# Optimization experiments

Hardware: AMD Instinct MI355X
Metric: run time of the kernel (lower is better)

Reference implementation:

```python
import jax, jax.numpy as jnp
import numpy as np

# Fixed geometry from the module's voxel_dict
VOXEL = np.array([0.32, 0.32, 6.0], dtype=np.float32)
PC_MIN = np.array([-74.88, -74.88, -2.0], dtype=np.float32)
PC_MAX = np.array([74.88, 74.88, 4.0], dtype=np.float32)
NX, NY, NZ = 468, 468, 1          # round((max-min)/voxel) per axis
CANVAS = NZ * NY * NX             # 219024 voxels (batch_size = 1)
OFFSET = VOXEL / 2.0 + PC_MIN     # x/y/z_offset from __init__


def setup_inputs() -> dict:
    key = jax.random.key(0)
    k1, k2, k3, k4 = jax.random.split(key, 4)
    N = 400000
    # points uniformly inside the point-cloud range (dynamic voxelization keeps all)
    xyz = jax.random.uniform(k1, (N, 3), dtype=jnp.float32) * (PC_MAX - PC_MIN) * 0.999 + PC_MIN
    extra = jax.random.normal(k2, (N, 2), dtype=jnp.float32)
    points = jnp.concatenate([xyz, extra], axis=1)          # [N, 5]
    W1 = jax.random.normal(k3, (11, 64), dtype=jnp.float32) * 0.05
    W2 = jax.random.normal(k4, (128, 64), dtype=jnp.float32) * 0.05
    return {"points": points, "W1": W1, "W2": W2}


def _flat_voxel_index(xyz):
    # dynamic voxelization: integer voxel coord per point, (z, y, x) ordering
    c = jnp.floor((xyz - PC_MIN) / VOXEL).astype(jnp.int32)
    cx = jnp.clip(c[:, 0], 0, NX - 1)
    cy = jnp.clip(c[:, 1], 0, NY - 1)
    cz = jnp.clip(c[:, 2], 0, NZ - 1)
    flat = cz * (NY * NX) + cy * NX + cx                    # canvas index as in map_voxel_center_to_point
    return flat, cx, cy, cz


def reference(points, W1, W2):
    xyz = points[:, :3]
    flat, cx, cy, cz = _flat_voxel_index(xyz)

    # DynamicScatter mean (cluster_scatter)
    cnt = jax.ops.segment_sum(jnp.ones((points.shape[0],), jnp.float32), flat, num_segments=CANVAS)
    vsum = jax.ops.segment_sum(points, flat, num_segments=CANVAS)
    vmean = vsum / jnp.maximum(cnt, 1.0)[:, None]           # [CANVAS, 5]
    pmean = vmean[flat]                                     # gather voxel mean to points

    f_cluster = xyz - pmean[:, :3]
    centers = jnp.stack([cx, cy, cz], axis=1).astype(jnp.float32) * VOXEL + OFFSET
    f_center = xyz - centers
    features = jnp.concatenate([points, f_cluster, f_center], axis=-1)   # [N, 11]

    occ = (cnt > 0)[:, None]

    # PFN layer 1: Linear(bias=False) + ReLU, then scatter-max to voxels
    pf1 = jax.nn.relu(features @ W1)                        # [N, 64]
    v1 = jax.ops.segment_max(pf1, flat, num_segments=CANVAS)
    v1 = jnp.where(occ, v1, 0.0)                            # zero empty voxels (replaces -inf)

    # gather voxel max back to points, concat, PFN layer 2
    feat2 = jnp.concatenate([pf1, v1[flat]], axis=1)        # [N, 128]
    pf2 = jax.nn.relu(feat2 @ W2)                           # [N, 64]
    v2 = jax.ops.segment_max(pf2, flat, num_segments=CANVAS)
    v2 = jnp.where(occ, v2, 0.0)                            # [CANVAS, 64] dense voxel features
    return v2
```

## Files before the change

kernel.cpp:

```cpp
#include <hip/hip_runtime.h>

#define NXc 468
#define NYc 468
#define CANVASc (468 * 468)
#define NPTS 400000
#define RUN 16
#define NRUNS (NPTS / RUN)
#define GPTS ((NPTS + 255) / 256)
#define GVOX ((CANVASc + 255) / 256)
#define GBND (NRUNS / 4)

#define PCMIN_X (-74.88f)
#define PCMIN_Y (-74.88f)
#define VOX_X 0.32f
#define VOX_Y 0.32f
#define OFF_X (-74.72f)
#define OFF_Y (-74.72f)
#define OFF_Z (1.0f)

typedef __attribute__((ext_vector_type(8))) short v8s;
typedef __attribute__((ext_vector_type(4))) float v4f;

static_assert(sizeof(__bf16) == 2, "bf16 must be 2 bytes");

__device__ __forceinline__ int rli(int x, int p) {
    return __builtin_amdgcn_readlane(x, p);
}
__device__ __forceinline__ float rlf(float x, int p) {
    return __int_as_float(__builtin_amdgcn_readlane(__float_as_int(x), p));
}

__device__ __forceinline__ void split8(const float* f, v8s& h, v8s& l) {
    #pragma unroll
    for (int i = 0; i < 8; i += 2) {
        __bf16 h0 = (__bf16)f[i];
        __bf16 h1 = (__bf16)f[i + 1];
        h[i]     = __builtin_bit_cast(short, h0);
        h[i + 1] = __builtin_bit_cast(short, h1);
        float l0 = f[i]     - (float)h0;
        float l1 = f[i + 1] - (float)h1;
        l[i]     = __builtin_bit_cast(short, (__bf16)l0);
        l[i + 1] = __builtin_bit_cast(short, (__bf16)l1);
    }
}

__device__ __forceinline__ int voxel_cell(float x, float y, int& cx, int& cy) {
    cx = (int)floorf((x - PCMIN_X) / VOX_X);
    cy = (int)floorf((y - PCMIN_Y) / VOX_Y);
    cx = min(max(cx, 0), NXc - 1);
    cy = min(max(cy, 0), NYc - 1);
    return cy * NXc + cx;
}

__device__ __forceinline__ void kw_body(int tid,
                                        const float* __restrict__ W1,
                                        const float* __restrict__ W2,
                                        v8s* __restrict__ w1frag,
                                        v8s* __restrict__ w2frag) {
    if (tid < 1024) {
        int f = tid >> 6, lane = tid & 63;
        int t = f >> 2, c = f & 3;
        int q = lane >> 4, n = lane & 15;
        float v[8];
        #pragma unroll
        for (int i = 0; i < 8; i++) v[i] = W2[(c * 32 + q * 8 + i) * 64 + t * 16 + n];
        v8s h, l;
        split8(v, h, l);
        w2frag[(f * 2 + 0) * 64 + lane] = h;
        w2frag[(f * 2 + 1) * 64 + lane] = l;
    } else if (tid < 1280) {
        int f = (tid - 1024) >> 6, lane = (tid - 1024) & 63;
        int q = lane >> 4, n = lane & 15;
        float v[8];
        #pragma unroll
        for (int i = 0; i < 8; i++) {
            int k = q * 8 + i;
            v[i] = (k < 11) ? W1[k * 64 + f * 16 + n] : 0.f;
        }
        v8s h, l;
        split8(v, h, l);
        w1frag[(f * 2 + 0) * 64 + lane] = h;
        w1frag[(f * 2 + 1) * 64 + lane] = l;
    }
}

__global__ __launch_bounds__(256) void k_stats(const float* __restrict__ pts,
                                               int* __restrict__ cnt,
                                               int* __restrict__ rankb,
                                               int* __restrict__ cellu,
                                               const float* __restrict__ W1,
                                               const float* __restrict__ W2,
                                               v8s* __restrict__ w1frag,
                                               v8s* __restrict__ w2frag) {
    int b = blockIdx.x;
    if (b >= GPTS) {
        kw_body((b - GPTS) * 256 + threadIdx.x, W1, W2, w1frag, w2frag);
        return;
    }
    int i = b * 256 + threadIdx.x;
    if (i >= NPTS) return;
    float x = pts[i * 5 + 0], y = pts[i * 5 + 1];
    int cx, cy;
    int fl = voxel_cell(x, y, cx, cy);
    rankb[i] = atomicAdd(&cnt[fl], 1);
    cellu[i] = cx | (cy << 16);
}

__global__ __launch_bounds__(256) void k_alloc(const int* __restrict__ cnt,
                                               int* __restrict__ cursor,
                                               int* __restrict__ gcur,
                                               float4* __restrict__ out4) {
    int v = blockIdx.x * 256 + threadIdx.x;
    int lane = threadIdx.x & 63;
    int c = (v < CANVASc) ? cnt[v] : 0;
    int scan = c;
    #pragma unroll
    for (int off = 1; off < 64; off <<= 1) {
        int t = __shfl_up(scan, off, 64);
        if (lane >= off) scan += t;
    }
    int total = __shfl(scan, 63, 64);
    int base = 0;
    if (lane == 0 && total > 0) base = atomicAdd(gcur, total);
    base = __shfl(base, 0, 64);
    if (v < CANVASc) {
        cursor[v] = base + scan - c;
        if (c == 0) {
            float4 z = make_float4(0.f, 0.f, 0.f, 0.f);
            float4* o = out4 + (size_t)v * 16;
            #pragma unroll
            for (int i = 0; i < 16; i++) o[i] = z;
        }
    }
}

__device__ __forceinline__ void gather_pt(const float* __restrict__ pts, int pi,
                                          float4& A, float& e1) {
    const float* pp = pts + (size_t)pi * 5;
    __builtin_memcpy(&A, pp, 16);
    e1 = pp[4];
}

__global__ __launch_bounds__(256) void k_scatter(const float* __restrict__ pts,
                                                 const int* __restrict__ cursor,
                                                 const int* __restrict__ rankb,
                                                 const int* __restrict__ cellu,
                                                 float4* __restrict__ pos4,
                                                 float* __restrict__ e1b,
                                                 int* __restrict__ cellb) {
    int i = blockIdx.x * 256 + threadIdx.x;
    if (i >= NPTS) return;
    float4 A; float e1;
    gather_pt(pts, i, A, e1);
    int cell = cellu[i];
    int cx = cell & 0xFFFF, cy = cell >> 16;
    int fl = cy * NXc + cx;
    int pos = cursor[fl] + rankb[i];
    pos4[pos] = A;
    e1b[pos] = e1;
    cellb[pos] = cell;
}

__global__ __launch_bounds__(256) void kS(const int* __restrict__ cnt,
                                          const int* __restrict__ cursor,
                                          const float4* __restrict__ pos4,
                                          const float* __restrict__ e1b,
                                          const int* __restrict__ cellb,
                                          const float* __restrict__ W1,
                                          float4* __restrict__ vmc,
                                          float* __restrict__ v1c,
                                          float* __restrict__ out) {
    int j = threadIdx.x & 63;
    int wslot = threadIdx.x >> 6;
    int w = blockIdx.x * 4 + wslot;
    if (w == 0 || w >= NRUNS) return;
    int bb = w * RUN;
    int ca = cellb[bb - 1], cb0 = cellb[bb];
    if (ca != cb0) return;
    int cx = ca & 0xFFFF, cy = ca >> 16;
    int v = cy * NXc + cx;
    int c = cnt[v];
    int start = cursor[v];
    out[(size_t)v * 64 + j] = 0.f;

    float sx = 0.f, sy = 0.f, sz = 0.f;
    for (int pb = 0; pb < c; pb += 64) {
        int pc = min(c - pb, 64);
        if (j < pc) {
            float4 A = pos4[start + pb + j];
            sx += A.x; sy += A.y; sz += A.z;
        }
    }
    #pragma unroll
    for (int off = 1; off < 64; off <<= 1) {
        sx += __shfl_xor(sx, off, 64);
        sy += __shfl_xor(sy, off, 64);
        sz += __shfl_xor(sz, off, 64);
    }
    float inv = 1.0f / (float)c;
    float mx = sx * inv, my = sy * inv, mz = sz * inv;
    if (j == 0) vmc[w] = make_float4(mx, my, mz, 0.f);

    float wgt[11];
    #pragma unroll
    for (int k = 0; k < 11; k++) wgt[k] = W1[k * 64 + j];
    float vmax = 0.f;
    for (int pb = 0; pb < c; pb += 64) {
        int pc = min(c - pb, 64);
        float f[11];
        #pragma unroll
        for (int k = 0; k < 11; k++) f[k] = 0.f;
        if (j < pc) {
            int idx = start + pb + j;
            float4 A = pos4[idx];
            float e1 = e1b[idx];
            int cell = cellb[idx];
            int ccx = cell & 0xFFFF, ccy = cell >> 16;
            f[0] = A.x; f[1] = A.y; f[2] = A.z; f[3] = A.w; f[4] = e1;
            f[5] = A.x - mx; f[6] = A.y - my; f[7] = A.z - mz;
            f[8] = A.x - (ccx * VOX_X + OFF_X);
            f[9] = A.y - (ccy * VOX_Y + OFF_Y);
            f[10] = A.z - OFF_Z;
        }
        for (int p = 0; p < pc; p++) {
            float acc = 0.f;
            #pragma unroll
            for (int k = 0; k < 11; k++)
                acc = fmaf(rlf(f[k], p), wgt[k], acc);
            vmax = fmaxf(vmax, acc);
        }
    }
    v1c[(size_t)w * 64 + j] = vmax;
}

struct PtRegs {
    float4 A;
    float  e1, fcx, fcy, fcz;
    float  mx, my, mz;
    int    vx;
};

#define PSTR 68

__device__ __forceinline__ void phase1_mfma(float (*s_pf)[PSTR], const PtRegs& P,
                                            const v8s* __restrict__ w1frag, int j) {
    if (j < RUN) {
        float* row = s_pf[j];
        row[0] = P.A.x; row[1] = P.A.y; row[2] = P.A.z; row[3] = P.A.w; row[4] = P.e1;
        row[5] = P.A.x - P.mx; row[6] = P.A.y - P.my; row[7] = P.A.z - P.mz;
        row[8] = P.fcx; row[9] = P.fcy; row[10] = P.fcz;
        #pragma unroll
        for (int t = 11; t < 16; t++) row[t] = 0.f;
    }
    __builtin_amdgcn_wave_barrier();

    const int m = j & 15, q = j >> 4;
    v8s fh = {0,0,0,0,0,0,0,0}, fl_ = {0,0,0,0,0,0,0,0};
    if (q < 2) {
        float f8[8];
        #pragma unroll
        for (int i = 0; i < 8; i++) f8[i] = s_pf[m][q * 8 + i];
        split8(f8, fh, fl_);
    }
    v4f d[4];
    #pragma unroll
    for (int t = 0; t < 4; t++) {
        v8s bh = w1frag[(t * 2 + 0) * 64 + j];
        v8s bl = w1frag[(t * 2 + 1) * 64 + j];
        v4f acc = {0.f, 0.f, 0.f, 0.f};
        acc = __builtin_amdgcn_mfma_f32_16x16x32_bf16(fh,  bh, acc, 0, 0, 0);
        acc = __builtin_amdgcn_mfma_f32_16x16x32_bf16(fl_, bh, acc, 0, 0, 0);
        acc = __builtin_amdgcn_mfma_f32_16x16x32_bf16(fh,  bl, acc, 0, 0, 0);
        d[t] = acc;
    }
    __builtin_amdgcn_wave_barrier();
    #pragma unroll
    for (int t = 0; t < 4; t++)
        #pragma unroll
        for (int r = 0; r < 4; r++)
            s_pf[q * 4 + r][t * 16 + m] = fmaxf(d[t][r], 0.f);
    __builtin_amdgcn_wave_barrier();
}

__global__ __launch_bounds__(256) void kB(const float4* __restrict__ pos4,
                                          const float* __restrict__ e1b,
                                          const int* __restrict__ cellb,
                                          const float4* __restrict__ vmc,
                                          const v8s* __restrict__ w1frag,
                                          const v8s* __restrict__ w2frag,
                                          const float* __restrict__ v1c,
                                          float* __restrict__ out) {
    __shared__ float s_pf[4][RUN][PSTR];
    int wslot = threadIdx.x >> 6;
    int wave = blockIdx.x * 4 + wslot;
    int j = threadIdx.x & 63;
    int base = wave * RUN;

    const int m = j & 15, q = j >> 4;

    int idx = -1;
    if (j < RUN) idx = base + j;
    else if (j == 16) idx = (base + RUN < NPTS) ? base + RUN : -1;
    else if (j == 17) idx = base - 1;

    int cell = 0, vx = -1;
    if (idx >= 0) {
        cell = cellb[idx];
        vx = (cell >> 16) * NXc + (cell & 0xFFFF);
    }
    float4 A = make_float4(0.f, 0.f, 0.f, 0.f);
    float e1 = 0.f;
    if (j < RUN) { A = pos4[idx]; e1 = e1b[idx]; }

    const int first = rli(vx, 0), last = rli(vx, RUN - 1);
    const bool firstExt = (rli(vx, 17) == first);
    const bool lastExt  = (rli(vx, 16) == last);

    int vx_m = __builtin_amdgcn_ds_bpermute(m << 2, vx);
    int vx_prev = __shfl_up(vx, 1, 64);
    unsigned long long B =
        __ballot((j < RUN) && ((j == 0) || (vx != vx_prev)));
    int s_seg = 63 - __builtin_clzll(B & ((2ULL << m) - 1ULL));
    int e_seg = m + 1 + (int)__builtin_ctzll((B | (1ULL << RUN)) >> (m + 1));
    const bool fext_m = (vx_m == first && firstExt);
    const bool ext_m = fext_m || (vx_m == last && lastExt);
    const int bidx = fext_m ? wave : (wave + 1);

    PtRegs P;
    P.A = A; P.e1 = e1; P.vx = vx;
    P.mx = P.my = P.mz = P.fcx = P.fcy = P.fcz = 0.f;
    if (j < RUN) {
        if (ext_m) {
            float4 mv = vmc[bidx];
            P.mx = mv.x; P.my = mv.y; P.mz = mv.z;
        } else {
            float sx = 0.f, sy = 0.f, sz = 0.f;
            for (int p = s_seg; p < e_seg; p++) {
                sx += __shfl(A.x, p, 64);
                sy += __shfl(A.y, p, 64);
                sz += __shfl(A.z, p, 64);
            }
            float inv = 1.0f / (float)(e_seg - s_seg);
            P.mx = sx * inv; P.my = sy * inv; P.mz = sz * inv;
        }
        int cx = cell & 0xFFFF, cy = cell >> 16;
        P.fcx = A.x - (cx * VOX_X + OFF_X);
        P.fcy = A.y - (cy * VOX_Y + OFF_Y);
        P.fcz = A.z - OFF_Z;
    }

    phase1_mfma(s_pf[wslot], P, w1frag, j);

    float vf[16];
    if (ext_m) {
        const float* vr = v1c + (size_t)bidx * 64 + q * 8;
        #pragma unroll
        for (int c = 0; c < 2; c++)
            #pragma unroll
            for (int i = 0; i < 8; i++) vf[c * 8 + i] = vr[c * 32 + i];
    }

    v8s ah[4], al[4];
    #pragma unroll
    for (int c = 0; c < 2; c++) {
        float f[8];
        #pragma unroll
        for (int i = 0; i < 8; i++) f[i] = s_pf[wslot][m][c * 32 + q * 8 + i];
        split8(f, ah[c], al[c]);
    }
    if (!ext_m) {
        #pragma unroll
        for (int i = 0; i < 16; i++) vf[i] = 0.f;
        for (int p = s_seg; p < e_seg; p++) {
            const float* row = s_pf[wslot][p];
            float4 a0 = *(const float4*)&row[q * 8];
            float4 a1 = *(const float4*)&row[q * 8 + 4];
            float4 b0 = *(const float4*)&row[32 + q * 8];
            float4 b1 = *(const float4*)&row[32 + q * 8 + 4];
            vf[0] = fmaxf(vf[0], a0.x);  vf[1] = fmaxf(vf[1], a0.y);
            vf[2] = fmaxf(vf[2], a0.z);  vf[3] = fmaxf(vf[3], a0.w);
            vf[4] = fmaxf(vf[4], a1.x);  vf[5] = fmaxf(vf[5], a1.y);
            vf[6] = fmaxf(vf[6], a1.z);  vf[7] = fmaxf(vf[7], a1.w);
            vf[8] = fmaxf(vf[8], b0.x);  vf[9] = fmaxf(vf[9], b0.y);
            vf[10] = fmaxf(vf[10], b0.z); vf[11] = fmaxf(vf[11], b0.w);
            vf[12] = fmaxf(vf[12], b1.x); vf[13] = fmaxf(vf[13], b1.y);
            vf[14] = fmaxf(vf[14], b1.z); vf[15] = fmaxf(vf[15], b1.w);
        }
    }
    split8(vf + 0, ah[2], al[2]);
    split8(vf + 8, ah[3], al[3]);
    __builtin_amdgcn_wave_barrier();

    #pragma unroll
    for (int t = 0; t < 4; t++) {
        v8s bh[4], bl[4];
        #pragma unroll
        for (int c = 0; c < 4; c++) {
            bh[c] = w2frag[((t * 4 + c) * 2 + 0) * 64 + j];
            bl[c] = w2frag[((t * 4 + c) * 2 + 1) * 64 + j];
        }
        v4f acc = {0.f, 0.f, 0.f, 0.f};
        #pragma unroll
        for (int c = 0; c < 4; c++) {
            acc = __builtin_amdgcn_mfma_f32_16x16x32_bf16(ah[c], bh[c], acc, 0, 0, 0);
            acc = __builtin_amdgcn_mfma_f32_16x16x32_bf16(al[c], bh[c], acc, 0, 0, 0);
            acc = __builtin_amdgcn_mfma_f32_16x16x32_bf16(ah[c], bl[c], acc, 0, 0, 0);
        }
        #pragma unroll
        for (int r = 0; r < 4; r++) s_pf[wslot][q * 4 + r][t * 16 + m] = acc[r];
    }
    __builtin_amdgcn_wave_barrier();

    int vprev = first;
    float smax = -3.4e38f;
    for (int p = 0; p < RUN; p++) {
        int vp = rli(vx, p);
        if (vp != vprev) {
            float r = fmaxf(smax, 0.f);
            size_t o = (size_t)vprev * 64 + j;
            bool ua = (vprev == first && firstExt) || (vprev == last && lastExt);
            if (ua) atomicMax((int*)out + o, __float_as_int(r));
            else out[o] = r;
            vprev = vp; smax = -3.4e38f;
        }
        smax = fmaxf(smax, s_pf[wslot][p][j]);
    }
    {
        float r = fmaxf(smax, 0.f);
        size_t o = (size_t)vprev * 64 + j;
        bool ua = (vprev == first && firstExt) || (vprev == last && lastExt);
        if (ua) atomicMax((int*)out + o, __float_as_int(r));
        else out[o] = r;
    }
}

extern "C" void kernel_launch(void* const* d_in, const int* in_sizes, int n_in,
                              void* d_out, int out_size, void* d_ws, size_t ws_size,
                              hipStream_t stream) {
    const float* pts = (const float*)d_in[0];
    const float* W1  = (const float*)d_in[1];
    const float* W2  = (const float*)d_in[2];
    float* out = (float*)d_out;

    float4* vmc    = (float4*)d_ws;
    float*  v1c    = (float*)(vmc + NRUNS);
    float4* pos4   = (float4*)(v1c + (size_t)NRUNS * 64);
    float*  e1b    = (float*)(pos4 + NPTS);
    int*    cellb  = (int*)(e1b + NPTS);
    int*    rankb  = cellb + NPTS;
    int*    cellu  = rankb + NPTS;
    v8s*    w2frag = (v8s*)(cellu + NPTS);
    v8s*    w1frag = w2frag + 2048;
    int*    cnt    = (int*)(w1frag + 512);
    int*    gcur   = cnt + CANVASc;
    int*    cursor = gcur + 1;

    hipMemsetAsync(cnt, 0, (size_t)(CANVASc + 1) * 4, stream);

    k_stats  <<<GPTS + 5, 256, 0, stream>>>(pts, cnt, rankb, cellu,
                                            W1, W2, w1frag, w2frag);
    k_alloc  <<<GVOX, 256, 0, stream>>>(cnt, cursor, gcur, (float4*)out);
    k_scatter<<<GPTS, 256, 0, stream>>>(pts, cursor, rankb, cellu,
                                        pos4, e1b, cellb);
    kS       <<<GBND, 256, 0, stream>>>(cnt, cursor, pos4, e1b, cellb,
                                        W1, vmc, v1c, out);
    kB       <<<NRUNS / 4, 256, 0, stream>>>(pos4, e1b, cellb, vmc, w1frag,
                                             w2frag, v1c, out);
}
```

Baseline: 223.4 us.

## Process two 16-point runs per wave in kB to reuse weight fragments

After: 218.0 us. 1.03x faster.

```diff
diff --git a/kernel.cpp b/kernel.cpp
--- a/kernel.cpp
+++ b/kernel.cpp
@@ -5,10 +5,13 @@
 #define CANVASc (468 * 468)
 #define NPTS 400000
 #define RUN 16
+#define WPTS 32
 #define NRUNS (NPTS / RUN)
+#define NWAVE (NPTS / WPTS)
 #define GPTS ((NPTS + 255) / 256)
 #define GVOX ((CANVASc + 255) / 256)
 #define GBND (NRUNS / 4)
+#define GKB  (NWAVE / 4)
 
 #define PCMIN_X (-74.88f)
 #define PCMIN_Y (-74.88f)
@@ -233,54 +236,7 @@
     v1c[(size_t)w * 64 + j] = vmax;
 }
 
-struct PtRegs {
-    float4 A;
-    float  e1, fcx, fcy, fcz;
-    float  mx, my, mz;
-    int    vx;
-};
-
 #define PSTR 68
-
-__device__ __forceinline__ void phase1_mfma(float (*s_pf)[PSTR], const PtRegs& P,
-                                            const v8s* __restrict__ w1frag, int j) {
-    if (j < RUN) {
-        float* row = s_pf[j];
-        row[0] = P.A.x; row[1] = P.A.y; row[2] = P.A.z; row[3] = P.A.w; row[4] = P.e1;
-        row[5] = P.A.x - P.mx; row[6] = P.A.y - P.my; row[7] = P.A.z - P.mz;
-        row[8] = P.fcx; row[9] = P.fcy; row[10] = P.fcz;
-        #pragma unroll
-        for (int t = 11; t < 16; t++) row[t] = 0.f;
-    }
-    __builtin_amdgcn_wave_barrier();
-
-    const int m = j & 15, q = j >> 4;
-    v8s fh = {0,0,0,0,0,0,0,0}, fl_ = {0,0,0,0,0,0,0,0};
-    if (q < 2) {
-        float f8[8];
-        #pragma unroll
-        for (int i = 0; i < 8; i++) f8[i] = s_pf[m][q * 8 + i];
-        split8(f8, fh, fl_);
-    }
-    v4f d[4];
-    #pragma unroll
-    for (int t = 0; t < 4; t++) {
-        v8s bh = w1frag[(t * 2 + 0) * 64 + j];
-        v8s bl = w1frag[(t * 2 + 1) * 64 + j];
-        v4f acc = {0.f, 0.f, 0.f, 0.f};
-        acc = __builtin_amdgcn_mfma_f32_16x16x32_bf16(fh,  bh, acc, 0, 0, 0);
-        acc = __builtin_amdgcn_mfma_f32_16x16x32_bf16(fl_, bh, acc, 0, 0, 0);
-        acc = __builtin_amdgcn_mfma_f32_16x16x32_bf16(fh,  bl, acc, 0, 0, 0);
-        d[t] = acc;
-    }
-    __builtin_amdgcn_wave_barrier();
-    #pragma unroll
-    for (int t = 0; t < 4; t++)
-        #pragma unroll
-        for (int r = 0; r < 4; r++)
-            s_pf[q * 4 + r][t * 16 + m] = fmaxf(d[t][r], 0.f);
-    __builtin_amdgcn_wave_barrier();
-}
 
 __global__ __launch_bounds__(256) void kB(const float4* __restrict__ pos4,
                                           const float* __restrict__ e1b,
@@ -290,18 +246,19 @@
                                           const v8s* __restrict__ w2frag,
                                           const float* __restrict__ v1c,
                                           float* __restrict__ out) {
-    __shared__ float s_pf[4][RUN][PSTR];
+    __shared__ float s_pf[4][WPTS][PSTR];
     int wslot = threadIdx.x >> 6;
     int wave = blockIdx.x * 4 + wslot;
     int j = threadIdx.x & 63;
-    int base = wave * RUN;
+    int base = wave * WPTS;
 
     const int m = j & 15, q = j >> 4;
+    float (*spf)[PSTR] = s_pf[wslot];
 
     int idx = -1;
-    if (j < RUN) idx = base + j;
-    else if (j == 16) idx = (base + RUN < NPTS) ? base + RUN : -1;
-    else if (j == 17) idx = base - 1;
+    if (j < WPTS) idx = base + j;
+    else if (j == 32) idx = (base + WPTS < NPTS) ? base + WPTS : -1;
+    else if (j == 33) idx = base - 1;
 
     int cell = 0, vx = -1;
     if (idx >= 0) {
@@ -310,85 +267,160 @@
     }
     float4 A = make_float4(0.f, 0.f, 0.f, 0.f);
     float e1 = 0.f;
-    if (j < RUN) { A = pos4[idx]; e1 = e1b[idx]; }
-
-    const int first = rli(vx, 0), last = rli(vx, RUN - 1);
-    const bool firstExt = (rli(vx, 17) == first);
-    const bool lastExt  = (rli(vx, 16) == last);
-
-    int vx_m = __builtin_amdgcn_ds_bpermute(m << 2, vx);
+    if (j < WPTS) { A = pos4[idx]; e1 = e1b[idx]; }
+
+    const int first0 = rli(vx, 0),  last0 = rli(vx, 15);
+    const int first1 = rli(vx, 16), last1 = rli(vx, 31);
+    const bool firstExt0 = (rli(vx, 33) == first0);
+    const bool midExt    = (first1 == last0);
+    const bool lastExt0  = midExt;
+    const bool firstExt1 = midExt;
+    const bool lastExt1  = (rli(vx, 32) == last1);
+
     int vx_prev = __shfl_up(vx, 1, 64);
     unsigned long long B =
-        __ballot((j < RUN) && ((j == 0) || (vx != vx_prev)));
-    int s_seg = 63 - __builtin_clzll(B & ((2ULL << m) - 1ULL));
-    int e_seg = m + 1 + (int)__builtin_ctzll((B | (1ULL << RUN)) >> (m + 1));
-    const bool fext_m = (vx_m == first && firstExt);
-    const bool ext_m = fext_m || (vx_m == last && lastExt);
-    const int bidx = fext_m ? wave : (wave + 1);
-
-    PtRegs P;
-    P.A = A; P.e1 = e1; P.vx = vx;
-    P.mx = P.my = P.mz = P.fcx = P.fcy = P.fcz = 0.f;
-    if (j < RUN) {
-        if (ext_m) {
-            float4 mv = vmc[bidx];
-            P.mx = mv.x; P.my = mv.y; P.mz = mv.z;
+        __ballot((j < WPTS) && ((j == 0) || (j == 16) || (vx != vx_prev)));
+
+    const int P1 = 16 + m;
+    int s0_ = 63 - __builtin_clzll(B & ((2ULL << m) - 1ULL));
+    int e0_ = m + 1 + (int)__builtin_ctzll((B | (1ULL << WPTS)) >> (m + 1));
+    int s1_ = 63 - __builtin_clzll(B & ((2ULL << P1) - 1ULL));
+    int e1_ = P1 + 1 + (int)__builtin_ctzll((B | (1ULL << WPTS)) >> (P1 + 1));
+
+    int vxm0 = __builtin_amdgcn_ds_bpermute(m << 2, vx);
+    int vxm1 = __builtin_amdgcn_ds_bpermute(P1 << 2, vx);
+    const bool fext0 = (vxm0 == first0 && firstExt0);
+    const bool ext0  = fext0 || (vxm0 == last0 && lastExt0);
+    const int  bidx0 = fext0 ? (2 * wave) : (2 * wave + 1);
+    const bool fext1 = (vxm1 == first1 && firstExt1);
+    const bool ext1  = fext1 || (vxm1 == last1 && lastExt1);
+    const int  bidx1 = fext1 ? (2 * wave + 1) : (2 * wave + 2);
+
+    float mx = 0.f, my = 0.f, mz = 0.f, fcx = 0.f, fcy = 0.f, fcz = 0.f;
+    if (j < WPTS) {
+        bool own_ext  = (j < 16) ? ext0 : ext1;
+        int  own_bidx = (j < 16) ? bidx0 : bidx1;
+        int  own_s    = (j < 16) ? s0_ : s1_;
+        int  own_e    = (j < 16) ? e0_ : e1_;
+        if (own_ext) {
+            float4 mv = vmc[own_bidx];
+            mx = mv.x; my = mv.y; mz = mv.z;
         } else {
             float sx = 0.f, sy = 0.f, sz = 0.f;
-            for (int p = s_seg; p < e_seg; p++) {
+            for (int p = own_s; p < own_e; p++) {
                 sx += __shfl(A.x, p, 64);
                 sy += __shfl(A.y, p, 64);
                 sz += __shfl(A.z, p, 64);
             }
-            float inv = 1.0f / (float)(e_seg - s_seg);
-            P.mx = sx * inv; P.my = sy * inv; P.mz = sz * inv;
+            float inv = 1.0f / (float)(own_e - own_s);
+            mx = sx * inv; my = sy * inv; mz = sz * inv;
         }
         int cx = cell & 0xFFFF, cy = cell >> 16;
-        P.fcx = A.x - (cx * VOX_X + OFF_X);
-        P.fcy = A.y - (cy * VOX_Y + OFF_Y);
-        P.fcz = A.z - OFF_Z;
-    }
-
-    phase1_mfma(s_pf[wslot], P, w1frag, j);
-
-    float vf[16];
-    if (ext_m) {
-        const float* vr = v1c + (size_t)bidx * 64 + q * 8;
+        fcx = A.x - (cx * VOX_X + OFF_X);
+        fcy = A.y - (cy * VOX_Y + OFF_Y);
+        fcz = A.z - OFF_Z;
+    }
+
+    if (j < WPTS) {
+        float* row = spf[j];
+        row[0] = A.x; row[1] = A.y; row[2] = A.z; row[3] = A.w; row[4] = e1;
+        row[5] = A.x - mx; row[6] = A.y - my; row[7] = A.z - mz;
+        row[8] = fcx; row[9] = fcy; row[10] = fcz;
+        #pragma unroll
+        for (int t = 11; t < 16; t++) row[t] = 0.f;
+    }
+    __builtin_amdgcn_wave_barrier();
+
+    v8s fh0 = {0,0,0,0,0,0,0,0}, fl0 = {0,0,0,0,0,0,0,0};
+    v8s fh1 = {0,0,0,0,0,0,0,0}, fl1 = {0,0,0,0,0,0,0,0};
+    if (q < 2) {
+        float f8[8];
+        #pragma unroll
+        for (int i = 0; i < 8; i++) f8[i] = spf[m][q * 8 + i];
+        split8(f8, fh0, fl0);
+        #pragma unroll
+        for (int i = 0; i < 8; i++) f8[i] = spf[16 + m][q * 8 + i];
+        split8(f8, fh1, fl1);
+    }
+    v4f d0[4], d1[4];
+    #pragma unroll
+    for (int t = 0; t < 4; t++) {
+        v8s bh = w1frag[(t * 2 + 0) * 64 + j];
+        v8s bl = w1frag[(t * 2 + 1) * 64 + j];
+        v4f a0 = {0.f, 0.f, 0.f, 0.f}, a1 = {0.f, 0.f, 0.f, 0.f};
+        a0 = __builtin_amdgcn_mfma_f32_16x16x32_bf16(fh0, bh, a0, 0, 0, 0);
+        a0 = __builtin_amdgcn_mfma_f32_16x16x32_bf16(fl0, bh, a0, 0, 0, 0);
+        a0 = __builtin_amdgcn_mfma_f32_16x16x32_bf16(fh0, bl, a0, 0, 0, 0);
+        a1 = __builtin_amdgcn_mfma_f32_16x16x32_bf16(fh1, bh, a1, 0, 0, 0);
+        a1 = __builtin_amdgcn_mfma_f32_16x16x32_bf16(fl1, bh, a1, 0, 0, 0);
+        a1 = __builtin_amdgcn_mfma_f32_16x16x32_bf16(fh1, bl, a1, 0, 0, 0);
+        d0[t] = a0; d1[t] = a1;
+    }
+    __builtin_amdgcn_wave_barrier();
+    #pragma unroll
+    for (int t = 0; t < 4; t++)
+        #pragma unroll
+        for (int r = 0; r < 4; r++) {
+            spf[q * 4 + r][t * 16 + m]      = fmaxf(d0[t][r], 0.f);
+            spf[16 + q * 4 + r][t * 16 + m] = fmaxf(d1[t][r], 0.f);
+        }
+    __builtin_amdgcn_wave_barrier();
+
+    float vf0[16], vf1[16];
+    if (ext0) {
+        const float* vr = v1c + (size_t)bidx0 * 64 + q * 8;
         #pragma unroll
         for (int c = 0; c < 2; c++)
             #pragma unroll
-            for (int i = 0; i < 8; i++) vf[c * 8 + i] = vr[c * 32 + i];
-    }
-
-    v8s ah[4], al[4];
+            for (int i = 0; i < 8; i++) vf0[c * 8 + i] = vr[c * 32 + i];
+    }
+    if (ext1) {
+        const float* vr = v1c + (size_t)bidx1 * 64 + q * 8;
+        #pragma unroll
+        for (int c = 0; c < 2; c++)
+            #pragma unroll
+            for (int i = 0; i < 8; i++) vf1[c * 8 + i] = vr[c * 32 + i];
+    }
+
+    v8s ah0[4], al0[4], ah1[4], al1[4];
     #pragma unroll
     for (int c = 0; c < 2; c++) {
         float f[8];
         #pragma unroll
-        for (int i = 0; i < 8; i++) f[i] = s_pf[wslot][m][c * 32 + q * 8 + i];
-        split8(f, ah[c], al[c]);
-    }
-    if (!ext_m) {
-        #pragma unroll
-        for (int i = 0; i < 16; i++) vf[i] = 0.f;
-        for (int p = s_seg; p < e_seg; p++) {
-            const float* row = s_pf[wslot][p];
-            float4 a0 = *(const float4*)&row[q * 8];
-            float4 a1 = *(const float4*)&row[q * 8 + 4];
-            float4 b0 = *(const float4*)&row[32 + q * 8];
-            float4 b1 = *(const float4*)&row[32 + q * 8 + 4];
-            vf[0] = fmaxf(vf[0], a0.x);  vf[1] = fmaxf(vf[1], a0.y);
-            vf[2] = fmaxf(vf[2], a0.z);  vf[3] = fmaxf(vf[3], a0.w);
-            vf[4] = fmaxf(vf[4], a1.x);  vf[5] = fmaxf(vf[5], a1.y);
-            vf[6] = fmaxf(vf[6], a1.z);  vf[7] = fmaxf(vf[7], a1.w);
-            vf[8] = fmaxf(vf[8], b0.x);  vf[9] = fmaxf(vf[9], b0.y);
-            vf[10] = fmaxf(vf[10], b0.z); vf[11] = fmaxf(vf[11], b0.w);
-            vf[12] = fmaxf(vf[12], b1.x); vf[13] = fmaxf(vf[13], b1.y);
-            vf[14] = fmaxf(vf[14], b1.z); vf[15] = fmaxf(vf[15], b1.w);
-        }
-    }
-    split8(vf + 0, ah[2], al[2]);
-    split8(vf + 8, ah[3], al[3]);
+        for (int i = 0; i < 8; i++) f[i] = spf[m][c * 32 + q * 8 + i];
+        split8(f, ah0[c], al0[c]);
+        #pragma unroll
+        for (int i = 0; i < 8; i++) f[i] = spf[16 + m][c * 32 + q * 8 + i];
+        split8(f, ah1[c], al1[c]);
+    }
+    if (!ext0) {
+        #pragma unroll
+        for (int i = 0; i < 16; i++) vf0[i] = 0.f;
+        for (int p = s0_; p < e0_; p++) {
+            const float* row = spf[p];
+            #pragma unroll
+            for (int i = 0; i < 8; i++) {
+                vf0[i]     = fmaxf(vf0[i],     row[q * 8 + i]);
+                vf0[8 + i] = fmaxf(vf0[8 + i], row[32 + q * 8 + i]);
+            }
+        }
+    }
+    if (!ext1) {
+        #pragma unroll
+        for (int i = 0; i < 16; i++) vf1[i] = 0.f;
+        for (int p = s1_; p < e1_; p++) {
+            const float* row = spf[p];
+            #pragma unroll
+            for (int i = 0; i < 8; i++) {
+                vf1[i]     = fmaxf(vf1[i],     row[q * 8 + i]);
+                vf1[8 + i] = fmaxf(vf1[8 + i], row[32 + q * 8 + i]);
+            }
+        }
+    }
+    split8(vf0 + 0, ah0[2], al0[2]);
+    split8(vf0 + 8, ah0[3], al0[3]);
+    split8(vf1 + 0, ah1[2], al1[2]);
+    split8(vf1 + 8, ah1[3], al1[3]);
     __builtin_amdgcn_wave_barrier();
 
     #pragma unroll
@@ -399,36 +431,67 @@
             bh[c] = w2frag[((t * 4 + c) * 2 + 0) * 64 + j];
             bl[c] = w2frag[((t * 4 + c) * 2 + 1) * 64 + j];
         }
-        v4f acc = {0.f, 0.f, 0.f, 0.f};
+        v4f a0 = {0.f, 0.f, 0.f, 0.f}, a1 = {0.f, 0.f, 0.f, 0.f};
         #pragma unroll
         for (int c = 0; c < 4; c++) {
-            acc = __builtin_amdgcn_mfma_f32_16x16x32_bf16(ah[c], bh[c], acc, 0, 0, 0);
-            acc = __builtin_amdgcn_mfma_f32_16x16x32_bf16(al[c], bh[c], acc, 0, 0, 0);
-            acc = __builtin_amdgcn_mfma_f32_16x16x32_bf16(ah[c], bl[c], acc, 0, 0, 0);
-        }
-        #pragma unroll
-        for (int r = 0; r < 4; r++) s_pf[wslot][q * 4 + r][t * 16 + m] = acc[r];
+            a0 = __builtin_amdgcn_mfma_f32_16x16x32_bf16(ah0[c], bh[c], a0, 0, 0, 0);
+            a0 = __builtin_amdgcn_mfma_f32_16x16x32_bf16(al0[c], bh[c], a0, 0, 0, 0);
+            a0 = __builtin_amdgcn_mfma_f32_16x16x32_bf16(ah0[c], bl[c], a0, 0, 0, 0);
+            a1 = __builtin_amdgcn_mfma_f32_16x16x32_bf16(ah1[c], bh[c], a1, 0, 0, 0);
+            a1 = __builtin_amdgcn_mfma_f32_16x16x32_bf16(al1[c], bh[c], a1, 0, 0, 0);
+            a1 = __builtin_amdgcn_mfma_f32_16x16x32_bf16(ah1[c], bl[c], a1, 0, 0, 0);
+        }
+        #pragma unroll
+        for (int r = 0; r < 4; r++) {
+            spf[q * 4 + r][t * 16 + m]      = a0[r];
+            spf[16 + q * 4 + r][t * 16 + m] = a1[r];
+        }
     }
     __builtin_amdgcn_wave_barrier();
 
-    int vprev = first;
-    float smax = -3.4e38f;
-    for (int p = 0; p < RUN; p++) {
-        int vp = rli(vx, p);
-        if (vp != vprev) {
-            float r = fmaxf(smax, 0.f);
-            size_t o = (size_t)vprev * 64 + j;
-            bool ua = (vprev == first && firstExt) || (vprev == last && lastExt);
-            if (ua) atomicMax((int*)out + o, __float_as_int(r));
-            else out[o] = r;
-            vprev = vp; smax = -3.4e38f;
-        }
-        smax = fmaxf(smax, s_pf[wslot][p][j]);
-    }
     {
+        int vprev = first0;
+        float smax = -3.4e38f;
+        for (int p = 0; p < 16; p++) {
+            int vp = rli(vx, p);
+            if (vp != vprev) {
+                float r = fmaxf(smax, 0.f);
+                size_t o = (size_t)vprev * 64 + j;
+                bool ua = (vprev == first0 && firstExt0) ||
+                          (vprev == last0 && lastExt0);
+                if (ua) atomicMax((int*)out + o, __float_as_int(r));
+                else out[o] = r;
+                vprev = vp; smax = -3.4e38f;
+            }
+            smax = fmaxf(smax, spf[p][j]);
+        }
         float r = fmaxf(smax, 0.f);
         size_t o = (size_t)vprev * 64 + j;
-        bool ua = (vprev == first && firstExt) || (vprev == last && lastExt);
+        bool ua = (vprev == first0 && firstExt0) ||
+                  (vprev == last0 && lastExt0);
+        if (ua) atomicMax((int*)out + o, __float_as_int(r));
+        else out[o] = r;
+    }
+    {
+        int vprev = first1;
+        float smax = -3.4e38f;
+        for (int p = 16; p < 32; p++) {
+            int vp = rli(vx, p);
+            if (vp != vprev) {
+                float r = fmaxf(smax, 0.f);
+                size_t o = (size_t)vprev * 64 + j;
+                bool ua = (vprev == first1 && firstExt1) ||
+                          (vprev == last1 && lastExt1);
+                if (ua) atomicMax((int*)out + o, __float_as_int(r));
+                else out[o] = r;
+                vprev = vp; smax = -3.4e38f;
+            }
+            smax = fmaxf(smax, spf[p][j]);
+        }
+        float r = fmaxf(smax, 0.f);
+        size_t o = (size_t)vprev * 64 + j;
+        bool ua = (vprev == first1 && firstExt1) ||
+                  (vprev == last1 && lastExt1);
         if (ua) atomicMax((int*)out + o, __float_as_int(r));
         else out[o] = r;
     }
@@ -464,6 +527,6 @@
                                         pos4, e1b, cellb);
     kS       <<<GBND, 256, 0, stream>>>(cnt, cursor, pos4, e1b, cellb,
                                         W1, vmc, v1c, out);
-    kB       <<<NRUNS / 4, 256, 0, stream>>>(pos4, e1b, cellb, vmc, w1frag,
-                                             w2frag, v1c, out);
-}
+    kB       <<<GKB, 256, 0, stream>>>(pos4, e1b, cellb, vmc, w1frag,
+                                       w2frag, v1c, out);
+}
```
